# Kernel optimization log

Hardware: AMD Instinct MI355X
Metric: run time of the kernel (lower is better)

The kernel has to match this reference:

```python
import jax, jax.numpy as jnp
import numpy as np

EPS = 1e-8
TAU = 0.2
IOU_THR = 0.5
NEG = -1e9
N, C, H, D_FG, D_CLS = 8192, 1024, 256, 64, 128


def setup_inputs() -> dict:
    key = jax.random.key(0)
    ks = jax.random.split(key, 11)
    def lin(k, fan_in, fan_out):
        return jax.random.normal(k, (fan_in, fan_out), jnp.float32) / np.sqrt(fan_in)
    return {
        "roi_feats": jax.random.normal(ks[0], (N, C), jnp.float32),
        "labels": jax.random.randint(ks[1], (N,), 0, 21, jnp.int32).astype(jnp.int64),
        "ious": jax.random.uniform(ks[2], (N,), jnp.float32),
        "fg_w1": lin(ks[3], C, H), "fg_b1": jnp.zeros((H,), jnp.float32),
        "fg_w2": lin(ks[4], H, D_FG), "fg_b2": jnp.zeros((D_FG,), jnp.float32),
        "cls_w1": lin(ks[5], C, H), "cls_b1": jnp.zeros((H,), jnp.float32),
        "cls_w2": lin(ks[6], H, D_CLS), "cls_b2": jnp.zeros((D_CLS,), jnp.float32),
    }


def _project_normalize(x, w1, b1, w2, b2):
    h = jax.nn.relu(x @ w1 + b1)
    z = h @ w2 + b2
    norm = jnp.maximum(jnp.linalg.norm(z, axis=1, keepdims=True), EPS)
    return z / norm


def _forward(roi_feats, labels, ious, fg_w1, fg_b1, fg_w2, fg_b2, cls_w1, cls_b1, cls_w2, cls_b2):
    n = roi_feats.shape[0]
    z_fg = _project_normalize(roi_feats, fg_w1, fg_b1, fg_w2, fg_b2)
    z_cls = _project_normalize(roi_feats, cls_w1, cls_b1, cls_w2, cls_b2)

    ignore = labels == -1
    fg = (labels > 0) & ~ignore
    iou_weight = jnp.where(ious > IOU_THR, ious, 0.0)
    eye = jnp.eye(n, dtype=bool)

    # ---- fg/bg contrastive (bg_as_negatives_only=True) ----
    sim_fg = (z_fg @ z_fg.T) / TAU                       # [N,N]
    exp_sim = jnp.exp(sim_fg)
    denom = jnp.sum(exp_sim * (~eye).astype(jnp.float32), axis=1)
    pos = (fg & ~ignore)[None, :] & ~eye                 # positives: fg columns, no self
    n_pos = jnp.sum(pos, axis=1)
    numer = jnp.sum(exp_sim * pos.astype(jnp.float32), axis=1)
    # original computes den = denom + EPS then -log((numer+EPS)/(den+EPS))
    loss_i = -jnp.log((numer + EPS) / (denom + 2.0 * EPS))
    valid = (fg & ~ignore) & (n_pos > 0)
    w = iou_weight * valid.astype(jnp.float32)
    loss_fg_bg = jnp.sum(w * loss_i) / (jnp.sum(w) + EPS)

    # ---- class supervised contrastive ----
    sim_cls = (z_cls @ z_cls.T) / TAU
    sim_masked = jnp.where(eye, NEG, sim_cls)
    log_denom = jax.nn.logsumexp(sim_masked, axis=1)     # [N]
    log_p = jnp.where(eye, NEG, sim_cls - log_denom[:, None])
    # pos_mask keeps diagonal (as in original): same label, col not ignore, col label != 0
    posc = (labels[None, :] == labels[:, None]) & (~ignore)[None, :] & (labels[None, :] != 0)
    n_posc = jnp.sum(posc, axis=1).astype(jnp.float32)
    sum_log_p = jnp.sum(log_p * posc.astype(jnp.float32), axis=1)
    valid_c = (fg & ~ignore) & (n_posc > 0) & jnp.isfinite(log_denom)
    Lzi = jnp.where(valid_c, -sum_log_p / (n_posc + EPS), 0.0)
    wc = iou_weight * valid_c.astype(jnp.float32)
    loss_supcon = jnp.sum(wc * Lzi) / (jnp.sum(wc) + EPS)

    return jnp.stack([loss_fg_bg, loss_supcon])


def reference(roi_feats, labels, ious, fg_w1, fg_b1, fg_w2, fg_b2, cls_w1, cls_b1, cls_w2, cls_b2):
    return _forward(roi_feats, labels, ious, fg_w1, fg_b1, fg_w2, fg_b2, cls_w1, cls_b1, cls_w2, cls_b2)
```

## Files before the change

kernel.cpp:

```cpp
#include <hip/hip_runtime.h>


typedef __attribute__((ext_vector_type(8))) short bs8;
typedef __attribute__((ext_vector_type(4))) float f4;

#define MFMA_BF16(a, b, c) __builtin_amdgcn_mfma_f32_16x16x32_bf16((a), (b), (c), 0, 0, 0)

#if defined(__has_builtin)
#if __has_builtin(__builtin_amdgcn_exp2f)
#define EXP2F(x) __builtin_amdgcn_exp2f(x)
#endif
#endif
#ifndef EXP2F
#define EXP2F(x) exp2f(x)
#endif

#define K_LOG2E 7.2134752044448170f

__device__ __forceinline__ unsigned short f2bf(float f) {
  unsigned int u = __float_as_uint(f);
  u = (u + 0x7fffu + ((u >> 16) & 1u)) >> 16;
  return (unsigned short)u;
}
__device__ __forceinline__ float bf2f(unsigned short s) {
  return __uint_as_float(((unsigned int)s) << 16);
}

constexpr size_t O_W1T  = 0;
constexpr size_t O_W2TF = 1048576;
constexpr size_t O_W2TC = 1081344;
constexpr size_t O_H    = 1146880;
constexpr size_t O_ZF   = 9535488;
constexpr size_t O_ZC   = 10584064;
constexpr size_t O_SCLS = 12681216;
constexpr size_t O_ROWD = 12697600;
constexpr size_t O_ROWN = 12730368;
constexpr size_t O_ROWS = 12763136;
constexpr size_t O_SCAL = 12795904;
constexpr size_t O_HIST = 12795920;
constexpr size_t O_NFG  = 12796048;
constexpr int ZERO_WORDS = (int)((O_SCAL + 16 - O_SCLS) / 4);

__global__ void __launch_bounds__(256) prep_kernel(
    const float* __restrict__ fgw1, const float* __restrict__ clsw1,
    const float* __restrict__ fgw2, const float* __restrict__ clsw2,
    const int* __restrict__ labels,
    unsigned short* __restrict__ W1T, unsigned short* __restrict__ W2Tf,
    unsigned short* __restrict__ W2Tc,
    int* __restrict__ hist, int* __restrict__ nfg, float* __restrict__ zp) {
  const int b = blockIdx.x;
  const int t = threadIdx.x;

  if (b >= 141) {
    const int i = (b - 141) * 256 + t;
    if (i < ZERO_WORDS) zp[i] = 0.f;
    return;
  }
  if (b == 140) {
    __shared__ int sh[33];
    if (t < 33) sh[t] = 0;
    __syncthreads();
    for (int it = 0; it < 32; it++) {
      const int lab = labels[it * 256 + t];
      if (lab >= 0 && lab < 32) atomicAdd(&sh[lab], 1);
      if (lab > 0) atomicAdd(&sh[32], 1);
    }
    __syncthreads();
    if (t < 32) hist[t] = sh[t];
    if (t == 32) *nfg = sh[32];
    return;
  }
  int m, tb;
  if (b < 64)       { m = 0; tb = b; }
  else if (b < 128) { m = 1; tb = b - 64; }
  else if (b < 132) { m = 2; tb = b - 128; }
  else              { m = 3; tb = b - 132; }
  __shared__ float tile[64][65];
  const float* src;
  unsigned short* dst;
  int R, C;
  if (m == 0)      { src = fgw1;  dst = W1T;              R = 1024; C = 256; }
  else if (m == 1) { src = clsw1; dst = W1T + 256 * 1024; R = 1024; C = 256; }
  else if (m == 2) { src = fgw2;  dst = W2Tf;             R = 256;  C = 64;  }
  else             { src = clsw2; dst = W2Tc;             R = 256;  C = 128; }
  const int cT = C >> 6;
  const int r0 = (tb / cT) << 6, c0 = (tb % cT) << 6;
  {
    const int rr = t >> 4, cc = (t & 15) << 2;
#pragma unroll
    for (int i = 0; i < 4; i++) {
      float4 v = *(const float4*)(src + (size_t)(r0 + rr + i * 16) * C + c0 + cc);
      tile[rr + i * 16][cc] = v.x; tile[rr + i * 16][cc + 1] = v.y;
      tile[rr + i * 16][cc + 2] = v.z; tile[rr + i * 16][cc + 3] = v.w;
    }
  }
  __syncthreads();
  {
    const int dr = t >> 2, dc = (t & 3) << 4;
    bs8 o0, o1;
#pragma unroll
    for (int j = 0; j < 8; j++) o0[j] = (short)f2bf(tile[dc + j][dr]);
#pragma unroll
    for (int j = 0; j < 8; j++) o1[j] = (short)f2bf(tile[dc + 8 + j][dr]);
    unsigned short* dp = dst + (size_t)(c0 + dr) * R + r0 + dc;
    *(bs8*)dp = o0;
    *(bs8*)(dp + 8) = o1;
  }
}

__global__ void __launch_bounds__(256) gemm1_kernel(
    const float* __restrict__ X, const unsigned short* __restrict__ W1T,
    const float* __restrict__ b1f, const float* __restrict__ b1c,
    unsigned short* __restrict__ H) {
  __shared__ __align__(16) unsigned short lA[64 * 40];
  __shared__ __align__(16) unsigned short lB[128 * 40];
  const int t = threadIdx.x;
  const int w = t >> 6, lane = t & 63, ln = lane & 15, quad = lane >> 4;
  const int m0 = blockIdx.x * 64, n0 = blockIdx.y * 128;

  f4 acc[8];
#pragma unroll
  for (int s = 0; s < 8; s++) acc[s] = (f4){0.f, 0.f, 0.f, 0.f};

  for (int k0 = 0; k0 < 1024; k0 += 32) {
    __syncthreads();
    {
      const int r = t >> 2, c = (t & 3) * 8;
      const float* xp = X + (size_t)(m0 + r) * 1024 + k0 + c;
      float4 x0 = *(const float4*)xp;
      float4 x1 = *(const float4*)(xp + 4);
      bs8 av;
      av[0] = (short)f2bf(x0.x); av[1] = (short)f2bf(x0.y);
      av[2] = (short)f2bf(x0.z); av[3] = (short)f2bf(x0.w);
      av[4] = (short)f2bf(x1.x); av[5] = (short)f2bf(x1.y);
      av[6] = (short)f2bf(x1.z); av[7] = (short)f2bf(x1.w);
      *(bs8*)&lA[r * 40 + c] = av;
    }
#pragma unroll
    for (int i = 0; i < 2; i++) {
      const int ch = t + i * 256;
      const int r = ch >> 2, c = (ch & 3) * 8;
      *(bs8*)&lB[r * 40 + c] = *(const bs8*)(W1T + (size_t)(n0 + r) * 1024 + k0 + c);
    }
    __syncthreads();
    bs8 af = *(const bs8*)&lA[(w * 16 + ln) * 40 + quad * 8];
#pragma unroll
    for (int s = 0; s < 8; s++) {
      bs8 bf = *(const bs8*)&lB[(s * 16 + ln) * 40 + quad * 8];
      acc[s] = MFMA_BF16(af, bf, acc[s]);
    }
  }
#pragma unroll
  for (int s = 0; s < 8; s++) {
    const int n = n0 + s * 16 + ln;
    const float b = (n < 256) ? b1f[n] : b1c[n - 256];
#pragma unroll
    for (int r = 0; r < 4; r++) {
      float v = fmaxf(acc[s][r] + b, 0.f);
      H[(size_t)(m0 + w * 16 + quad * 4 + r) * 512 + n] = f2bf(v);
    }
  }
}

__global__ void __launch_bounds__(256) gemm2_kernel(
    const unsigned short* __restrict__ H,
    const unsigned short* __restrict__ W2Tf, const unsigned short* __restrict__ W2Tc,
    const float* __restrict__ b2f, const float* __restrict__ b2c,
    unsigned short* __restrict__ Zf, unsigned short* __restrict__ Zc) {
  const int t = threadIdx.x;
  const int w = t >> 6, lane = t & 63, ln = lane & 15, quad = lane >> 4;
  const int rw = blockIdx.x * 32 + (w & 1) * 16;

  if (w < 2) {
    const unsigned short* hrow = H + (size_t)(rw + ln) * 512;
    f4 acc[4];
#pragma unroll
    for (int s = 0; s < 4; s++) acc[s] = (f4){0.f, 0.f, 0.f, 0.f};
#pragma unroll
    for (int ks = 0; ks < 8; ks++) {
      bs8 af = *(const bs8*)(hrow + ks * 32 + quad * 8);
#pragma unroll
      for (int s = 0; s < 4; s++) {
        bs8 bf = *(const bs8*)(W2Tf + (size_t)(s * 16 + ln) * 256 + ks * 32 + quad * 8);
        acc[s] = MFMA_BF16(af, bf, acc[s]);
      }
    }
    float ss[4] = {0.f, 0.f, 0.f, 0.f};
#pragma unroll
    for (int s = 0; s < 4; s++) {
      float b = b2f[s * 16 + ln];
#pragma unroll
      for (int r = 0; r < 4; r++) {
        acc[s][r] += b;
        ss[r] = fmaf(acc[s][r], acc[s][r], ss[r]);
      }
    }
#pragma unroll
    for (int r = 0; r < 4; r++) {
#pragma unroll
      for (int off = 1; off < 16; off <<= 1) ss[r] += __shfl_xor(ss[r], off, 64);
      float sc = 1.f / fmaxf(sqrtf(ss[r]), 1e-8f);
#pragma unroll
      for (int s = 0; s < 4; s++)
        Zf[(size_t)(rw + quad * 4 + r) * 64 + s * 16 + ln] = f2bf(acc[s][r] * sc);
    }
  } else {
    const unsigned short* hrow = H + (size_t)(rw + ln) * 512 + 256;
    f4 acc[8];
#pragma unroll
    for (int s = 0; s < 8; s++) acc[s] = (f4){0.f, 0.f, 0.f, 0.f};
#pragma unroll
    for (int ks = 0; ks < 8; ks++) {
      bs8 af = *(const bs8*)(hrow + ks * 32 + quad * 8);
#pragma unroll
      for (int s = 0; s < 8; s++) {
        bs8 bf = *(const bs8*)(W2Tc + (size_t)(s * 16 + ln) * 256 + ks * 32 + quad * 8);
        acc[s] = MFMA_BF16(af, bf, acc[s]);
      }
    }
    float ss[4] = {0.f, 0.f, 0.f, 0.f};
#pragma unroll
    for (int s = 0; s < 8; s++) {
      float b = b2c[s * 16 + ln];
#pragma unroll
      for (int r = 0; r < 4; r++) {
        acc[s][r] += b;
        ss[r] = fmaf(acc[s][r], acc[s][r], ss[r]);
      }
    }
#pragma unroll
    for (int r = 0; r < 4; r++) {
#pragma unroll
      for (int off = 1; off < 16; off <<= 1) ss[r] += __shfl_xor(ss[r], off, 64);
      float sc = 1.f / fmaxf(sqrtf(ss[r]), 1e-8f);
#pragma unroll
      for (int s = 0; s < 8; s++)
        Zc[(size_t)(rw + quad * 4 + r) * 128 + s * 16 + ln] = f2bf(acc[s][r] * sc);
    }
  }
}

__global__ void __launch_bounds__(128) scls_kernel(const unsigned short* __restrict__ Zc,
                                                   const int* __restrict__ labels,
                                                   float* __restrict__ Scls) {
  const int c = blockIdx.x + 1;
  const int t = threadIdx.x;
  const int r0 = blockIdx.y * 256;
  float acc = 0.f;
#pragma unroll 4
  for (int r = r0; r < r0 + 256; r++) {
    if (labels[r] == c) acc += bf2f(Zc[(size_t)r * 128 + t]);
  }
  atomicAdd(&Scls[c * 128 + t], acc);
}

__global__ void __launch_bounds__(256) simfg_kernel(
    const unsigned short* __restrict__ Zf, const int* __restrict__ labels,
    float* __restrict__ rowD, float* __restrict__ rowN) {
  const int bi = blockIdx.x, d = blockIdx.y;
  if (d == 32 && bi >= 32) return;
  const int bj = (bi + d) & 63;
  const bool diag = (d == 0);

  __shared__ __align__(16) unsigned short sZf[64 * 72];
  __shared__ float sFg[64];
  __shared__ float sCol[4][2][4][16][2];
  const int t = threadIdx.x;
  const int w = t >> 6, lane = t & 63, ln = lane & 15, quad = lane >> 4;
  const int rbase = bi * 128 + w * 32;

  bs8 afg[2][2];
  float fgr[2][4];
#pragma unroll
  for (int rs = 0; rs < 2; rs++) {
    const unsigned short* zf = Zf + (size_t)(rbase + rs * 16 + ln) * 64;
#pragma unroll
    for (int s = 0; s < 2; s++) afg[rs][s] = *(const bs8*)(zf + s * 32 + quad * 8);
#pragma unroll
    for (int r = 0; r < 4; r++)
      fgr[rs][r] = (labels[rbase + rs * 16 + quad * 4 + r] > 0) ? 1.f : 0.f;
  }

  float dacc[2][4] = {}, nacc[2][4] = {};
  float cd[2][4] = {}, cn[2][4] = {};

#pragma unroll
  for (int ct = 0; ct < 2; ct++) {
    const int c0 = bj * 128 + ct * 64;
    __syncthreads();
#pragma unroll
    for (int i = 0; i < 2; i++) {
      int ch = t + i * 256;
      int j = ch >> 3, c8 = (ch & 7) * 8;
      *(bs8*)&sZf[j * 72 + c8] = *(const bs8*)(Zf + (size_t)(c0 + j) * 64 + c8);
    }
    if (t < 64) sFg[t] = (labels[c0 + t] > 0) ? 1.f : 0.f;
    __syncthreads();

#pragma unroll
    for (int s = 0; s < 4; s++) {
      const int lcol = s * 16 + ln;
      const float fgc = sFg[lcol];
      bs8 b0 = *(const bs8*)&sZf[lcol * 72 + quad * 8];
      bs8 b1 = *(const bs8*)&sZf[lcol * 72 + 32 + quad * 8];
#pragma unroll
      for (int rs = 0; rs < 2; rs++) {
        f4 c = {0.f, 0.f, 0.f, 0.f};
        c = MFMA_BF16(afg[rs][0], b0, c);
        c = MFMA_BF16(afg[rs][1], b1, c);
#pragma unroll
        for (int r = 0; r < 4; r++) {
          float e = EXP2F(c[r] * K_LOG2E);
          dacc[rs][r] += e;
          nacc[rs][r] = fmaf(fgc, e, nacc[rs][r]);
          cd[ct][s] += e;
          cn[ct][s] = fmaf(fgr[rs][r], e, cn[ct][s]);
        }
      }
    }
  }

  if (!diag) {
#pragma unroll
    for (int ct = 0; ct < 2; ct++)
#pragma unroll
      for (int s = 0; s < 4; s++) {
        float dv = cd[ct][s], nv = cn[ct][s];
#pragma unroll
        for (int off = 16; off < 64; off <<= 1) {
          dv += __shfl_xor(dv, off, 64);
          nv += __shfl_xor(nv, off, 64);
        }
        if (quad == 0) {
          sCol[w][ct][s][ln][0] = dv;
          sCol[w][ct][s][ln][1] = nv;
        }
      }
    __syncthreads();
    if (t < 128) {
      const int ct = t >> 6, s = (t >> 4) & 3, lm = t & 15;
      float dv = 0.f, nv = 0.f;
#pragma unroll
      for (int ww = 0; ww < 4; ww++) {
        dv += sCol[ww][ct][s][lm][0];
        nv += sCol[ww][ct][s][lm][1];
      }
      const int col = bj * 128 + t;
      atomicAdd(&rowD[col], dv);
      atomicAdd(&rowN[col], nv);
    }
  }

#pragma unroll
  for (int rs = 0; rs < 2; rs++)
#pragma unroll
    for (int r = 0; r < 4; r++) {
      float dv = dacc[rs][r], nv = nacc[rs][r];
#pragma unroll
      for (int off = 1; off < 16; off <<= 1) {
        dv += __shfl_xor(dv, off, 64);
        nv += __shfl_xor(nv, off, 64);
      }
      if (ln == 0) {
        int row = rbase + rs * 16 + quad * 4 + r;
        atomicAdd(&rowD[row], dv);
        atomicAdd(&rowN[row], nv);
      }
    }
}

__global__ void __launch_bounds__(256) simcls_kernel(
    const unsigned short* __restrict__ Zc, float* __restrict__ rowS) {
  const int bi = blockIdx.x, d = blockIdx.y;
  if (d == 32 && bi >= 32) return;
  const int bj = (bi + d) & 63;
  const bool diag = (d == 0);

  __shared__ __align__(16) unsigned short sZc[64 * 136];
  __shared__ float sCol[4][2][4][16];
  const int t = threadIdx.x;
  const int w = t >> 6, lane = t & 63, ln = lane & 15, quad = lane >> 4;
  const int rbase = bi * 128 + w * 32;

  bs8 acl[2][4];
#pragma unroll
  for (int rs = 0; rs < 2; rs++) {
    const unsigned short* zc = Zc + (size_t)(rbase + rs * 16 + ln) * 128;
#pragma unroll
    for (int s = 0; s < 4; s++) acl[rs][s] = *(const bs8*)(zc + s * 32 + quad * 8);
  }

  float sacc[2][4] = {};
  float cs[2][4] = {};

#pragma unroll
  for (int ct = 0; ct < 2; ct++) {
    const int c0 = bj * 128 + ct * 64;
    __syncthreads();
#pragma unroll
    for (int i = 0; i < 4; i++) {
      int ch = t + i * 256;
      int j = ch >> 4, c8 = (ch & 15) * 8;
      *(bs8*)&sZc[j * 136 + c8] = *(const bs8*)(Zc + (size_t)(c0 + j) * 128 + c8);
    }
    __syncthreads();

#pragma unroll
    for (int s = 0; s < 4; s++) {
      const int lcol = s * 16 + ln;
      bs8 bc0 = *(const bs8*)&sZc[lcol * 136 + quad * 8];
      bs8 bc1 = *(const bs8*)&sZc[lcol * 136 + 32 + quad * 8];
      bs8 bc2 = *(const bs8*)&sZc[lcol * 136 + 64 + quad * 8];
      bs8 bc3 = *(const bs8*)&sZc[lcol * 136 + 96 + quad * 8];
#pragma unroll
      for (int rs = 0; rs < 2; rs++) {
        f4 c = {0.f, 0.f, 0.f, 0.f};
        c = MFMA_BF16(acl[rs][0], bc0, c);
        c = MFMA_BF16(acl[rs][1], bc1, c);
        c = MFMA_BF16(acl[rs][2], bc2, c);
        c = MFMA_BF16(acl[rs][3], bc3, c);
#pragma unroll
        for (int r = 0; r < 4; r++) {
          float e = EXP2F(c[r] * K_LOG2E);
          sacc[rs][r] += e;
          cs[ct][s] += e;
        }
      }
    }
  }

  if (!diag) {
#pragma unroll
    for (int ct = 0; ct < 2; ct++)
#pragma unroll
      for (int s = 0; s < 4; s++) {
        float sv = cs[ct][s];
#pragma unroll
        for (int off = 16; off < 64; off <<= 1) sv += __shfl_xor(sv, off, 64);
        if (quad == 0) sCol[w][ct][s][ln] = sv;
      }
    __syncthreads();
    if (t < 128) {
      const int ct = t >> 6, s = (t >> 4) & 3, lm = t & 15;
      float sv = 0.f;
#pragma unroll
      for (int ww = 0; ww < 4; ww++) sv += sCol[ww][ct][s][lm];
      atomicAdd(&rowS[bj * 128 + t], sv);
    }
  }

#pragma unroll
  for (int rs = 0; rs < 2; rs++)
#pragma unroll
    for (int r = 0; r < 4; r++) {
      float sv = sacc[rs][r];
#pragma unroll
      for (int off = 1; off < 16; off <<= 1) sv += __shfl_xor(sv, off, 64);
      if (ln == 0)
        atomicAdd(&rowS[rbase + rs * 16 + quad * 4 + r], sv);
    }
}

__global__ void __launch_bounds__(256) finalize_kernel(
    const unsigned short* __restrict__ Zf, const unsigned short* __restrict__ Zc,
    const int* __restrict__ labels, const float* __restrict__ ious,
    const float* __restrict__ rowD, const float* __restrict__ rowN,
    const float* __restrict__ rowS, const float* __restrict__ Scls,
    const int* __restrict__ hist, const int* __restrict__ nfg,
    float* __restrict__ scal) {
  __shared__ float red[4][4];
  const int t = threadIdx.x, w = t >> 6, lane = t & 63;
  float aw0 = 0.f, al0 = 0.f, aw1 = 0.f, al1 = 0.f;
  const int NFG = *nfg;
  for (int it = 0; it < 16; it++) {
    const int i = it * 512 + blockIdx.x * 4 + w;
    const int lab = labels[i];
    if (lab > 0 && lab < 32) {
      const float iou = ious[i];
      const float iw = (iou > 0.5f) ? iou : 0.f;
      float dot = 0.f, ssq = 0.f;
#pragma unroll
      for (int p = 0; p < 2; p++) {
        const int k = lane + p * 64;
        const float z = bf2f(Zc[(size_t)i * 128 + k]);
        dot = fmaf(z, Scls[lab * 128 + k], dot);
        ssq = fmaf(z, z, ssq);
      }
      float zf = bf2f(Zf[(size_t)i * 64 + lane]);
      float ssqf = zf * zf;
#pragma unroll
      for (int off = 1; off < 64; off <<= 1) {
        dot += __shfl_xor(dot, off, 64);
        ssq += __shfl_xor(ssq, off, 64);
        ssqf += __shfl_xor(ssqf, off, 64);
      }
      if (lane == 0) {
        const float ef = EXP2F(K_LOG2E * ssqf);
        if (NFG - 1 > 0) {
          const float D = rowD[i] - ef;
          const float Nn = rowN[i] - ef;
          const float loss = logf(D + 2e-8f) - logf(Nn + 1e-8f);
          aw0 += iw;
          al0 += iw * loss;
        }
        const int npc = hist[lab];
        if (npc > 0) {
          const float S = rowS[i] - EXP2F(K_LOG2E * ssq);
          const float logden = logf(S);
          const float slp = (dot - ssq) * 5.0f - (float)(npc - 1) * logden - 1e9f;
          aw1 += iw;
          al1 += iw * (-slp / ((float)npc + 1e-8f));
        }
      }
    }
  }
  if (lane == 0) { red[w][0] = aw0; red[w][1] = al0; red[w][2] = aw1; red[w][3] = al1; }
  __syncthreads();
  if (t < 4) atomicAdd(&scal[t], red[0][t] + red[1][t] + red[2][t] + red[3][t]);
}

__global__ void writeout_kernel(const float* __restrict__ scal, float* __restrict__ out) {
  if (threadIdx.x == 0) {
    out[0] = scal[1] / (scal[0] + 1e-8f);
    out[1] = scal[3] / (scal[2] + 1e-8f);
  }
}

extern "C" void kernel_launch(void* const* d_in, const int* in_sizes, int n_in,
                              void* d_out, int out_size, void* d_ws, size_t ws_size,
                              hipStream_t stream) {
  (void)in_sizes; (void)n_in; (void)out_size; (void)ws_size;
  const float* roi    = (const float*)d_in[0];
  const int*   labels = (const int*)d_in[1];
  const float* ious   = (const float*)d_in[2];
  const float* fgw1   = (const float*)d_in[3];
  const float* fgb1   = (const float*)d_in[4];
  const float* fgw2   = (const float*)d_in[5];
  const float* fgb2   = (const float*)d_in[6];
  const float* clsw1  = (const float*)d_in[7];
  const float* clsb1  = (const float*)d_in[8];
  const float* clsw2  = (const float*)d_in[9];
  const float* clsb2  = (const float*)d_in[10];

  char* ws = (char*)d_ws;
  unsigned short* W1T  = (unsigned short*)(ws + O_W1T);
  unsigned short* W2Tf = (unsigned short*)(ws + O_W2TF);
  unsigned short* W2Tc = (unsigned short*)(ws + O_W2TC);
  unsigned short* Hb   = (unsigned short*)(ws + O_H);
  unsigned short* Zf   = (unsigned short*)(ws + O_ZF);
  unsigned short* Zc   = (unsigned short*)(ws + O_ZC);
  float* Scls = (float*)(ws + O_SCLS);
  float* rowD = (float*)(ws + O_ROWD);
  float* rowN = (float*)(ws + O_ROWN);
  float* rowS = (float*)(ws + O_ROWS);
  float* scal = (float*)(ws + O_SCAL);
  int* hist = (int*)(ws + O_HIST);
  int* nfg  = (int*)(ws + O_NFG);
  float* out = (float*)d_out;

  hipLaunchKernelGGL(prep_kernel, dim3(254), dim3(256), 0, stream,
                     fgw1, clsw1, fgw2, clsw2, labels, W1T, W2Tf, W2Tc,
                     hist, nfg, (float*)(ws + O_SCLS));
  hipLaunchKernelGGL(gemm1_kernel, dim3(128, 4), dim3(256), 0, stream,
                     roi, W1T, fgb1, clsb1, Hb);
  hipLaunchKernelGGL(gemm2_kernel, dim3(256), dim3(256), 0, stream,
                     Hb, W2Tf, W2Tc, fgb2, clsb2, Zf, Zc);
  hipLaunchKernelGGL(scls_kernel, dim3(20, 32), dim3(128), 0, stream, Zc, labels, Scls);
  hipLaunchKernelGGL(simfg_kernel, dim3(64, 33), dim3(256), 0, stream,
                     Zf, labels, rowD, rowN);
  hipLaunchKernelGGL(simcls_kernel, dim3(64, 33), dim3(256), 0, stream, Zc, rowS);
  hipLaunchKernelGGL(finalize_kernel, dim3(128), dim3(256), 0, stream,
                     Zf, Zc, labels, ious, rowD, rowN, rowS, Scls, hist, nfg, scal);
  hipLaunchKernelGGL(writeout_kernel, dim3(1), dim3(64), 0, stream, scal, out);
}
```

Before: 220.3 us.

## Prefetch next K-tile into registers and widen gemm1 K-step to 64

The first projection GEMM now loads the next 64-wide K slice of X and W1T into registers while MFMAs run on the current LDS tile, instead of loading and then immediately waiting each iteration. The K step doubles from 32 to 64, halving the number of barrier pairs and loop iterations, and the LDS row pitch grows to 72. The cost is more live registers per thread for the prefetch buffers and larger shared memory use, which could lower occupancy.

```diff
diff --git a/kernel.cpp b/kernel.cpp
--- a/kernel.cpp
+++ b/kernel.cpp
@@ -112,43 +112,62 @@
     const float* __restrict__ X, const unsigned short* __restrict__ W1T,
     const float* __restrict__ b1f, const float* __restrict__ b1c,
     unsigned short* __restrict__ H) {
-  __shared__ __align__(16) unsigned short lA[64 * 40];
-  __shared__ __align__(16) unsigned short lB[128 * 40];
+  __shared__ __align__(16) unsigned short lA[64 * 72];
+  __shared__ __align__(16) unsigned short lB[128 * 72];
   const int t = threadIdx.x;
   const int w = t >> 6, lane = t & 63, ln = lane & 15, quad = lane >> 4;
   const int m0 = blockIdx.x * 64, n0 = blockIdx.y * 128;
 
+  const int ar = t >> 2, ac = (t & 3) * 16;
+  const int br = t >> 1, bc = (t & 1) * 32;
+  const float* xbase = X + (size_t)(m0 + ar) * 1024 + ac;
+  const unsigned short* bbase = W1T + (size_t)(n0 + br) * 1024 + bc;
+
+  float4 xa[4];
+  bs8 xb[4];
+#pragma unroll
+  for (int i = 0; i < 4; i++) xa[i] = *(const float4*)(xbase + i * 4);
+#pragma unroll
+  for (int i = 0; i < 4; i++) xb[i] = *(const bs8*)(bbase + i * 8);
+
   f4 acc[8];
 #pragma unroll
   for (int s = 0; s < 8; s++) acc[s] = (f4){0.f, 0.f, 0.f, 0.f};
 
-  for (int k0 = 0; k0 < 1024; k0 += 32) {
-    __syncthreads();
+  for (int ks = 0; ks < 16; ks++) {
     {
-      const int r = t >> 2, c = (t & 3) * 8;
-      const float* xp = X + (size_t)(m0 + r) * 1024 + k0 + c;
-      float4 x0 = *(const float4*)xp;
-      float4 x1 = *(const float4*)(xp + 4);
-      bs8 av;
-      av[0] = (short)f2bf(x0.x); av[1] = (short)f2bf(x0.y);
-      av[2] = (short)f2bf(x0.z); av[3] = (short)f2bf(x0.w);
-      av[4] = (short)f2bf(x1.x); av[5] = (short)f2bf(x1.y);
-      av[6] = (short)f2bf(x1.z); av[7] = (short)f2bf(x1.w);
-      *(bs8*)&lA[r * 40 + c] = av;
-    }
-#pragma unroll
-    for (int i = 0; i < 2; i++) {
-      const int ch = t + i * 256;
-      const int r = ch >> 2, c = (ch & 3) * 8;
-      *(bs8*)&lB[r * 40 + c] = *(const bs8*)(W1T + (size_t)(n0 + r) * 1024 + k0 + c);
-    }
-    __syncthreads();
-    bs8 af = *(const bs8*)&lA[(w * 16 + ln) * 40 + quad * 8];
-#pragma unroll
-    for (int s = 0; s < 8; s++) {
-      bs8 bf = *(const bs8*)&lB[(s * 16 + ln) * 40 + quad * 8];
-      acc[s] = MFMA_BF16(af, bf, acc[s]);
-    }
+      unsigned short* ap = &lA[ar * 72 + ac];
+#pragma unroll
+      for (int i = 0; i < 2; i++) {
+        bs8 av;
+        av[0] = (short)f2bf(xa[2 * i].x);     av[1] = (short)f2bf(xa[2 * i].y);
+        av[2] = (short)f2bf(xa[2 * i].z);     av[3] = (short)f2bf(xa[2 * i].w);
+        av[4] = (short)f2bf(xa[2 * i + 1].x); av[5] = (short)f2bf(xa[2 * i + 1].y);
+        av[6] = (short)f2bf(xa[2 * i + 1].z); av[7] = (short)f2bf(xa[2 * i + 1].w);
+        *(bs8*)(ap + i * 8) = av;
+      }
+      unsigned short* bp = &lB[br * 72 + bc];
+#pragma unroll
+      for (int i = 0; i < 4; i++) *(bs8*)(bp + i * 8) = xb[i];
+    }
+    __syncthreads();
+    if (ks < 15) {
+      const int k1 = (ks + 1) * 64;
+#pragma unroll
+      for (int i = 0; i < 4; i++) xa[i] = *(const float4*)(xbase + k1 + i * 4);
+#pragma unroll
+      for (int i = 0; i < 4; i++) xb[i] = *(const bs8*)(bbase + k1 + i * 8);
+    }
+#pragma unroll
+    for (int kk = 0; kk < 2; kk++) {
+      bs8 af = *(const bs8*)&lA[(w * 16 + ln) * 72 + kk * 32 + quad * 8];
+#pragma unroll
+      for (int s = 0; s < 8; s++) {
+        bs8 bf = *(const bs8*)&lB[(s * 16 + ln) * 72 + kk * 32 + quad * 8];
+        acc[s] = MFMA_BF16(af, bf, acc[s]);
+      }
+    }
+    __syncthreads();
   }
 #pragma unroll
   for (int s = 0; s < 8; s++) {
```

Measured after the change: 212.4 us. 1.04x faster.
